# Kernel optimization log

Measured on AMD Instinct MI355X. Metric: run time of the kernel, lower is better.

The kernel has to match this reference:

```python
import jax, jax.numpy as jnp
import numpy as np

B, Nq, Nk, R = 4, 1024, 1024, 256
NH, DK, DV = 8, 64, 64


def setup_inputs() -> dict:
    key = jax.random.key(0)
    ks = jax.random.split(key, 16)
    mk = lambda k, shape, s=1.0: jax.random.normal(k, shape, dtype=jnp.float32) * s
    inp = {
        'Q_real': mk(ks[0], (B, Nq, R)), 'Q_imag': mk(ks[1], (B, Nq, R)),
        'K_real': mk(ks[2], (B, Nk, R)), 'K_imag': mk(ks[3], (B, Nk, R)),
        'V_real': mk(ks[4], (B, Nk, R)), 'V_imag': mk(ks[5], (B, Nk, R)),
        'WQ_r': mk(ks[6], (NH * DK, R), 0.02), 'WQ_i': mk(ks[7], (NH * DK, R), 0.02),
        'WK_r': mk(ks[8], (NH * DK, R), 0.02), 'WK_i': mk(ks[9], (NH * DK, R), 0.02),
        'WV_r': mk(ks[10], (NH * DV, R), 0.02), 'WV_i': mk(ks[11], (NH * DV, R), 0.02),
        'WO_r': mk(ks[12], (R, NH * DV), 0.02), 'WO_i': mk(ks[13], (R, NH * DV), 0.02),
        'mask': jax.random.randint(ks[14], (B, Nk), 0, 2).astype(bool),
    }
    return inp


def _complex_linear(x, w_r, w_i):
    # x: complex [..., in]; weights real [out, in]. Same math as 4 real matmuls.
    w = (w_r + 1j * w_i).astype(jnp.complex64)
    return x @ w.T


def reference(Q_real, Q_imag, K_real, K_imag, V_real, V_imag,
              WQ_r, WQ_i, WK_r, WK_i, WV_r, WV_i, WO_r, WO_i, mask):
    Q = (Q_real + 1j * Q_imag).astype(jnp.complex64)
    K = (K_real + 1j * K_imag).astype(jnp.complex64)
    V = (V_real + 1j * V_imag).astype(jnp.complex64)

    Qp = _complex_linear(Q, WQ_r, WQ_i).reshape(B, Nq, NH, DK).transpose(0, 2, 1, 3)
    Kp = _complex_linear(K, WK_r, WK_i).reshape(B, Nk, NH, DK).transpose(0, 2, 1, 3)
    Vp = _complex_linear(V, WV_r, WV_i).reshape(B, Nk, NH, DV).transpose(0, 2, 1, 3)

    # complex scores [B, NH, Nq, Nk]; conj on K matches torch .conj().transpose
    scores = jnp.einsum('bhqd,bhkd->bhqk', Qp, jnp.conj(Kp)) / jnp.sqrt(jnp.float32(DK))
    scores_abs = jnp.abs(scores)

    m = mask[:, None, None, :]                    # [B,1,1,Nk]
    valid = jnp.any(mask, axis=-1)[:, None, None, None]  # [B,1,1,1] valid query rows
    masked = jnp.where(m, scores_abs, -jnp.inf)
    # avoid all -inf rows feeding softmax (those rows are zeroed afterwards)
    safe = jnp.where(valid, masked, 0.0)
    w = jax.nn.softmax(safe, axis=-1)
    w = jnp.where(valid, w, 0.0)

    attn = jnp.einsum('bhqk,bhkd->bhqd', w.astype(Vp.dtype), Vp)
    attn = attn.transpose(0, 2, 1, 3).reshape(B, Nq, NH * DV)
    return _complex_linear(attn, WO_r, WO_i)
```

## Files before the change

kernel.cpp:

```cpp
#include <hip/hip_runtime.h>
#include <math.h>

#define NBATCH 4
#define NSEQ   1024
#define RD     256
#define NHEAD  8
#define HD     64
#define NHD    512

typedef __attribute__((ext_vector_type(8))) short  short8;
typedef __attribute__((ext_vector_type(4))) short  short4v;
typedef __attribute__((ext_vector_type(4))) float  float4v;

#define MFMA16(a,b,c) __builtin_amdgcn_mfma_f32_16x16x32_bf16(a,b,c,0,0,0)

typedef const void __attribute__((address_space(1)))* gas_t;
typedef void __attribute__((address_space(3)))* las_t;
#define GLOAD16(g, l) __builtin_amdgcn_global_load_lds((gas_t)(g), (las_t)(l), 16, 0, 0)

static __device__ __forceinline__ unsigned short f2b(float f) {
    union { float f; unsigned u; } x; x.f = f;
    unsigned r = x.u + 0x7fffu + ((x.u >> 16) & 1u);
    return (unsigned short)(r >> 16);
}
static __device__ __forceinline__ void st4(short* dst, float4v v) {
    short4v p;
    p[0] = (short)f2b(v[0]); p[1] = (short)f2b(v[1]);
    p[2] = (short)f2b(v[2]); p[3] = (short)f2b(v[3]);
    *(short4v*)dst = p;
}

__global__ __launch_bounds__(1024) void mask_norm(
    const void* __restrict__ mraw, unsigned char* __restrict__ nm)
{
    __shared__ int isByteLayout;
    const int t = threadIdx.x;
    if (t == 0) isByteLayout = 0;
    __syncthreads();
    const int* mi = (const int*)mraw;
    int v = mi[t];
    if (v & ~1) isByteLayout = 1;
    __syncthreads();
    const unsigned char* mb = (const unsigned char*)mraw;
    if (isByteLayout) {
        #pragma unroll
        for (int j = 0; j < 4; j++) { int k = t*4 + j; nm[k] = mb[k] ? 1 : 0; }
    } else {
        #pragma unroll
        for (int j = 0; j < 4; j++) { int k = t*4 + j; nm[k] = mi[k] ? 1 : 0; }
    }
}

struct ConvArgs { const float* src[14]; short* dst[14]; int n4[14]; };

__global__ __launch_bounds__(256) void convert_bf16(ConvArgs ca)
{
    const int a = blockIdx.y;
    const float* __restrict__ s = ca.src[a];
    short* __restrict__ d = ca.dst[a];
    const int n4 = ca.n4[a];
    for (int i = blockIdx.x*256 + threadIdx.x; i < n4; i += gridDim.x*256) {
        float4v v = *(const float4v*)(s + (size_t)i*4);
        st4(d + (size_t)i*4, v);
    }
}

struct ProjArgs {
    const short* Xr[3]; const short* Xi[3];
    const short* Wr[3]; const short* Wi[3];
    short* Yr[3]; short* Yi[3];
};

__global__ __launch_bounds__(256) void cgemm_proj(ProjArgs pa)
{
    __shared__ short sX[2][64][64];
    __shared__ short sW[2][64][64];
    const int z = blockIdx.z;
    const short* __restrict__ X_r = pa.Xr[z];
    const short* __restrict__ X_i = pa.Xi[z];
    const short* __restrict__ W_r = pa.Wr[z];
    const short* __restrict__ W_i = pa.Wi[z];
    short* __restrict__ Y_r = pa.Yr[z];
    short* __restrict__ Y_i = pa.Yi[z];
    const int transposeOut = (z == 2);

    const int tid  = threadIdx.x;
    const int lane = tid & 63, wave = tid >> 6;
    const int quad = lane >> 4, l16 = lane & 15;
    const int sw8  = l16 & 7;
    const int rsub = lane >> 3;
    const int colg = (lane & 7) ^ rsub;
    const int n0 = blockIdx.x * 64, m0 = blockIdx.y * 64;

    const short nk = (short)0x8000;
    const short8 neg = {nk,nk,nk,nk,nk,nk,nk,nk};

    float4v zf = {0.f,0.f,0.f,0.f};
    float4v Yr[4], Yi[4];
    #pragma unroll
    for (int t = 0; t < 4; t++) { Yr[t] = zf; Yi[t] = zf; }

    for (int kc = 0; kc < RD; kc += 64) {
        __syncthreads();
        {
            const short* gp; short* lp; int rbase;
            if      (wave == 0) { gp = X_r; lp = &sX[0][0][0]; rbase = m0; }
            else if (wave == 1) { gp = X_i; lp = &sX[1][0][0]; rbase = m0; }
            else if (wave == 2) { gp = W_r; lp = &sW[0][0][0]; rbase = n0; }
            else                { gp = W_i; lp = &sW[1][0][0]; rbase = n0; }
            #pragma unroll
            for (int j = 0; j < 8; j++) {
                int row = j*8 + rsub;
                GLOAD16(gp + (size_t)(rbase + row)*RD + kc + colg*8, lp + j*512);
            }
        }
        __syncthreads();
        short8 fxr[2], fxi[2], fxin[2];
        #pragma unroll
        for (int ds = 0; ds < 2; ds++) {
            int u = ((ds*4 + quad) ^ sw8) * 8;
            fxr[ds]  = *(short8*)&sX[0][wave*16 + l16][u];
            fxi[ds]  = *(short8*)&sX[1][wave*16 + l16][u];
            fxin[ds] = fxi[ds] ^ neg;
        }
        #pragma unroll
        for (int t = 0; t < 4; t++)
            #pragma unroll
            for (int ds = 0; ds < 2; ds++) {
                int u = ((ds*4 + quad) ^ sw8) * 8;
                short8 wr = *(short8*)&sW[0][t*16 + l16][u];
                short8 wi = *(short8*)&sW[1][t*16 + l16][u];
                Yr[t] = MFMA16(fxr[ds],  wr, Yr[t]);
                Yr[t] = MFMA16(fxin[ds], wi, Yr[t]);
                Yi[t] = MFMA16(fxr[ds],  wi, Yi[t]);
                Yi[t] = MFMA16(fxi[ds],  wr, Yi[t]);
            }
    }

    const int b = m0 >> 10, h = n0 >> 6, nb = m0 & 1023;
    short* sT = &sX[0][0][0];
    short* Yp[2] = { Y_r, Y_i };
    #pragma unroll
    for (int p = 0; p < 2; p++) {
        __syncthreads();
        #pragma unroll
        for (int t = 0; t < 4; t++)
            #pragma unroll
            for (int r = 0; r < 4; r++) {
                float v = p ? Yi[t][r] : Yr[t][r];
                int rr = wave*16 + quad*4 + r;
                int cc = t*16 + l16;
                if (!transposeOut) sT[rr*68 + cc] = (short)f2b(v);
                else               sT[cc*68 + rr] = (short)f2b(v);
            }
        __syncthreads();
        #pragma unroll
        for (int it = 0; it < 2; it++) {
            int idx = it*256 + tid;
            int rr = idx >> 3, c8 = (idx & 7)*8;
            short4v a = *(short4v*)&sT[rr*68 + c8];
            short4v bq = *(short4v*)&sT[rr*68 + c8 + 4];
            short8 v8 = { a[0],a[1],a[2],a[3], bq[0],bq[1],bq[2],bq[3] };
            size_t o = transposeOut
                ? (((size_t)(b*NHEAD + h))*HD + rr)*NSEQ + nb + c8
                : (((size_t)(b*NHEAD + h))*NSEQ + nb + rr)*HD + c8;
            *(short8*)&Yp[p][o] = v8;
        }
    }
}

__global__ __launch_bounds__(256) void attn_mfma(
    const short* __restrict__ Qp_r, const short* __restrict__ Qp_i,
    const short* __restrict__ Kp_r, const short* __restrict__ Kp_i,
    const short* __restrict__ Vp_r, const short* __restrict__ Vp_i,
    const unsigned char* __restrict__ mask,
    short* __restrict__ Ar, short* __restrict__ Ai)
{
    __shared__ short sK[2][64][64];
    __shared__ short sV[2][64][64];
    __shared__ short sP[4][16][72];
    __shared__ unsigned char smask[1024];

    const int tid  = threadIdx.x;
    const int lane = tid & 63, wave = tid >> 6;
    const int quad = lane >> 4, l16 = lane & 15;
    const int sw8  = l16 & 7;
    const int qt = blockIdx.x & 15;
    const int bh = blockIdx.x >> 4;
    const int b  = bh >> 3, h = bh & 7;
    const size_t base = (size_t)bh * (NSEQ*HD);

    const int rsub = lane >> 3;
    const int colg = (lane & 7) ^ rsub;

    ((int*)smask)[tid] = ((const int*)(mask + b*NSEQ))[tid];

    {
        const int q0 = qt*64;
        #pragma unroll
        for (int j = 0; j < 4; j++) {
            int c = wave*4 + j;
            const short* gp = (c >> 3) ? Qp_i : Qp_r;
            short* lp = (c >> 3) ? &sK[1][0][0] : &sK[0][0][0];
            int jj = c & 7;
            int row = jj*8 + rsub;
            GLOAD16(gp + base + (size_t)(q0 + row)*HD + colg*8, lp + jj*512);
        }
    }
    __syncthreads();

    short8 fqr[2], fqi[2], fqrn[2];
    {
        const short nk = (short)0x8000;
        short8 neg = {nk,nk,nk,nk,nk,nk,nk,nk};
        const int qrow = wave*16 + l16;
        #pragma unroll
        for (int ds = 0; ds < 2; ds++) {
            int u = ((ds*4 + quad) ^ sw8) * 8;
            fqr[ds]  = *(short8*)&sK[0][qrow][u];
            fqi[ds]  = *(short8*)&sK[1][qrow][u];
            fqrn[ds] = fqr[ds] ^ neg;
        }
    }

    float4v zf = {0.f,0.f,0.f,0.f};
    float4v Or[4], Oi[4];
    float lrow[4];
    #pragma unroll
    for (int t = 0; t < 4; t++) { Or[t] = zf; Oi[t] = zf; }
    #pragma unroll
    for (int r = 0; r < 4; r++) lrow[r] = 0.f;

    const float C2 = 0.18033688f;

    for (int kt = 0; kt < 16; kt++) {
        const int k0 = kt*64;
        __syncthreads();
        {
            const short* gp; short* lp; int isV;
            if      (wave == 0) { gp = Kp_r; lp = &sK[0][0][0]; isV = 0; }
            else if (wave == 1) { gp = Kp_i; lp = &sK[1][0][0]; isV = 0; }
            else if (wave == 2) { gp = Vp_r; lp = &sV[0][0][0]; isV = 1; }
            else                { gp = Vp_i; lp = &sV[1][0][0]; isV = 1; }
            #pragma unroll
            for (int j = 0; j < 8; j++) {
                int row = j*8 + rsub;
                const short* g = isV
                    ? gp + base + (size_t)row*NSEQ + k0 + colg*8
                    : gp + base + (size_t)(k0 + row)*HD + colg*8;
                GLOAD16(g, lp + j*512);
            }
        }
        __syncthreads();

        float4v Sr[4], Si[4];
        #pragma unroll
        for (int t = 0; t < 4; t++) { Sr[t] = zf; Si[t] = zf; }
        #pragma unroll
        for (int t = 0; t < 4; t++)
            #pragma unroll
            for (int ds = 0; ds < 2; ds++) {
                int u = ((ds*4 + quad) ^ sw8) * 8;
                short8 kr = *(short8*)&sK[0][t*16 + l16][u];
                short8 ki = *(short8*)&sK[1][t*16 + l16][u];
                Sr[t] = MFMA16(fqr[ds],  kr, Sr[t]);
                Sr[t] = MFMA16(fqi[ds],  ki, Sr[t]);
                Si[t] = MFMA16(fqi[ds],  kr, Si[t]);
                Si[t] = MFMA16(fqrn[ds], ki, Si[t]);
            }

        #pragma unroll
        for (int t = 0; t < 4; t++) {
            bool mv = smask[k0 + t*16 + l16] != 0;
            #pragma unroll
            for (int r = 0; r < 4; r++) {
                float a = Sr[t][r], c = Si[t][r];
                float x = fmaf(a, a, c*c);
                float s = __builtin_amdgcn_sqrtf(x);
                float e = mv ? __builtin_amdgcn_exp2f(C2 * s) : 0.f;
                lrow[r] += e;
                sP[wave][quad*4 + r][t*16 + l16] = (short)f2b(e);
            }
        }

        #pragma unroll
        for (int ks = 0; ks < 2; ks++) {
            short8 fp = *(short8*)&sP[wave][l16][ks*32 + quad*8];
            #pragma unroll
            for (int t = 0; t < 4; t++) {
                int u = ((ks*4 + quad) ^ sw8) * 8;
                short8 vr = *(short8*)&sV[0][t*16 + l16][u];
                short8 vi = *(short8*)&sV[1][t*16 + l16][u];
                Or[t] = MFMA16(fp, vr, Or[t]);
                Oi[t] = MFMA16(fp, vi, Oi[t]);
            }
        }
    }

    float inv[4];
    #pragma unroll
    for (int r = 0; r < 4; r++) {
        float ls = lrow[r];
        ls += __shfl_xor(ls, 1, 64);
        ls += __shfl_xor(ls, 2, 64);
        ls += __shfl_xor(ls, 4, 64);
        ls += __shfl_xor(ls, 8, 64);
        inv[r] = (ls > 0.f) ? 1.f/ls : 0.f;
    }
    #pragma unroll
    for (int t = 0; t < 4; t++)
        #pragma unroll
        for (int r = 0; r < 4; r++) {
            int q = qt*64 + wave*16 + quad*4 + r;
            int d = t*16 + l16;
            size_t o = ((size_t)(b*NSEQ + q))*NHD + h*HD + d;
            Ar[o] = (short)f2b(Or[t][r] * inv[r]);
            Ai[o] = (short)f2b(Oi[t][r] * inv[r]);
        }
}

__global__ __launch_bounds__(256) void cgemm_out(
    const short* __restrict__ A_r, const short* __restrict__ A_i,
    const short* __restrict__ W_r, const short* __restrict__ W_i,
    float* __restrict__ Out, int writeImagPlane)
{
    __shared__ short sA[2][64][64];
    __shared__ short sW[2][32][64];
    const int tid  = threadIdx.x;
    const int lane = tid & 63, wave = tid >> 6;
    const int quad = lane >> 4, l16 = lane & 15;
    const int sw8  = l16 & 7;
    const int rsub = lane >> 3;
    const int colg = (lane & 7) ^ rsub;
    const int n0 = blockIdx.x * 32, m0 = blockIdx.y * 64;

    const short nk = (short)0x8000;
    const short8 neg = {nk,nk,nk,nk,nk,nk,nk,nk};

    float4v zf = {0.f,0.f,0.f,0.f};
    float4v Yr[2], Yi[2];
    #pragma unroll
    for (int t = 0; t < 2; t++) { Yr[t] = zf; Yi[t] = zf; }

    for (int kc = 0; kc < NHD; kc += 64) {
        __syncthreads();
        {
            if (wave < 2) {
                const short* gp = wave ? A_i : A_r;
                short* lp = wave ? &sA[1][0][0] : &sA[0][0][0];
                #pragma unroll
                for (int j = 0; j < 8; j++) {
                    int row = j*8 + rsub;
                    GLOAD16(gp + (size_t)(m0 + row)*NHD + kc + colg*8, lp + j*512);
                }
            } else {
                const short* gp = (wave == 3) ? W_i : W_r;
                short* lp = (wave == 3) ? &sW[1][0][0] : &sW[0][0][0];
                #pragma unroll
                for (int j = 0; j < 4; j++) {
                    int row = j*8 + rsub;
                    GLOAD16(gp + (size_t)(n0 + row)*NHD + kc + colg*8, lp + j*512);
                }
            }
        }
        __syncthreads();
        short8 far[2], fai[2], fain[2];
        #pragma unroll
        for (int ds = 0; ds < 2; ds++) {
            int u = ((ds*4 + quad) ^ sw8) * 8;
            far[ds]  = *(short8*)&sA[0][wave*16 + l16][u];
            fai[ds]  = *(short8*)&sA[1][wave*16 + l16][u];
            fain[ds] = fai[ds] ^ neg;
        }
        #pragma unroll
        for (int t = 0; t < 2; t++)
            #pragma unroll
            for (int ds = 0; ds < 2; ds++) {
                int u = ((ds*4 + quad) ^ sw8) * 8;
                short8 wr = *(short8*)&sW[0][t*16 + l16][u];
                short8 wi = *(short8*)&sW[1][t*16 + l16][u];
                Yr[t] = MFMA16(far[ds],  wr, Yr[t]);
                Yr[t] = MFMA16(fain[ds], wi, Yr[t]);
                Yi[t] = MFMA16(far[ds],  wi, Yi[t]);
                Yi[t] = MFMA16(fai[ds],  wr, Yi[t]);
            }
    }
    const size_t TOT = (size_t)NBATCH * NSEQ * RD;
    #pragma unroll
    for (int t = 0; t < 2; t++)
        #pragma unroll
        for (int r = 0; r < 4; r++) {
            int row = m0 + wave*16 + quad*4 + r;
            int col = n0 + t*16 + l16;
            size_t o = (size_t)row*RD + col;
            Out[o] = Yr[t][r];
            if (writeImagPlane) Out[o + TOT] = Yi[t][r];
        }
}

extern "C" void kernel_launch(void* const* d_in, const int* in_sizes, int n_in,
                              void* d_out, int out_size, void* d_ws, size_t ws_size,
                              hipStream_t stream)
{
    float* out = (float*)d_out;

    const size_t P = (size_t)NBATCH * NHEAD * NSEQ * HD;
    const size_t H = (size_t)NBATCH * NSEQ * RD;
    const size_t WSZ = (size_t)NHD * RD;

    short* bws = (short*)d_ws;
    short* Qpr = bws + 0*P;  short* Qpi = bws + 1*P;
    short* Kpr = bws + 2*P;  short* Kpi = bws + 3*P;
    short* Vpr = bws + 4*P;  short* Vpi = bws + 5*P;
    short* conv = bws + 6*P;
    short* cX[6]; for (int i = 0; i < 6; i++) cX[i] = conv + i*H;
    short* cW[6]; for (int i = 0; i < 6; i++) cW[i] = conv + 6*H + i*WSZ;
    short* cWOr = conv + 6*H + 6*WSZ;
    short* cWOi = conv + 6*H + 7*WSZ;
    short* Apr = conv;
    short* Api = conv + P;
    unsigned char* nmask = (unsigned char*)(conv + 6*H + 8*WSZ);

    const size_t TOT = (size_t)NBATCH * NSEQ * RD;
    const int writeImagPlane = ((size_t)out_size >= 2*TOT) ? 1 : 0;

    ConvArgs ca;
    for (int i = 0; i < 6; i++) {
        ca.src[i] = (const float*)d_in[i];  ca.dst[i] = cX[i];  ca.n4[i] = (int)(H/4);
    }
    for (int i = 0; i < 6; i++) {
        ca.src[6+i] = (const float*)d_in[6+i]; ca.dst[6+i] = cW[i]; ca.n4[6+i] = (int)(WSZ/4);
    }
    ca.src[12] = (const float*)d_in[12]; ca.dst[12] = cWOr; ca.n4[12] = (int)(WSZ/4);
    ca.src[13] = (const float*)d_in[13]; ca.dst[13] = cWOi; ca.n4[13] = (int)(WSZ/4);

    ProjArgs pa;
    pa.Xr[0] = cX[0]; pa.Xi[0] = cX[1];
    pa.Xr[1] = cX[2]; pa.Xi[1] = cX[3];
    pa.Xr[2] = cX[4]; pa.Xi[2] = cX[5];
    pa.Wr[0] = cW[0]; pa.Wi[0] = cW[1];
    pa.Wr[1] = cW[2]; pa.Wi[1] = cW[3];
    pa.Wr[2] = cW[4]; pa.Wi[2] = cW[5];
    pa.Yr[0] = Qpr; pa.Yi[0] = Qpi;
    pa.Yr[1] = Kpr; pa.Yi[1] = Kpi;
    pa.Yr[2] = Vpr; pa.Yi[2] = Vpi;

    mask_norm<<<1, 1024, 0, stream>>>(d_in[14], nmask);
    convert_bf16<<<dim3(256, 14), 256, 0, stream>>>(ca);
    cgemm_proj<<<dim3(8, 64, 3), 256, 0, stream>>>(pa);
    attn_mfma<<<dim3(512), 256, 0, stream>>>(Qpr, Qpi, Kpr, Kpi, Vpr, Vpi,
                                             nmask, Apr, Api);
    cgemm_out<<<dim3(8, 64), 256, 0, stream>>>(Apr, Api, cWOr, cWOi, out,
                                               writeImagPlane);
}
```

Before: 176.3 us.

## Fold mask normalization into convert kernel, enlarge projection M-tile, reorder attention blocks

Removes the separate mask_norm launch by handling the mask as an extra y-slice of convert_bf16, saving one kernel launch. The projection GEMM now uses 128-row M tiles, with each wave computing two 16-row sub-tiles, so every loaded W tile is reused twice and the grid is halved. The attention grid mapping is reordered so consecutive blocks cover different batch-heads rather than query tiles of the same head. The larger GEMM tile raises register and LDS use and lowers block count, which may reduce occupancy.

New measurement: 175.4 us. No clear change (-0.5%).

```diff
diff --git a/kernel.cpp b/kernel.cpp
--- a/kernel.cpp
+++ b/kernel.cpp
@@ -30,32 +30,35 @@
     *(short4v*)dst = p;
 }
 
-__global__ __launch_bounds__(1024) void mask_norm(
-    const void* __restrict__ mraw, unsigned char* __restrict__ nm)
-{
-    __shared__ int isByteLayout;
-    const int t = threadIdx.x;
-    if (t == 0) isByteLayout = 0;
-    __syncthreads();
-    const int* mi = (const int*)mraw;
-    int v = mi[t];
-    if (v & ~1) isByteLayout = 1;
-    __syncthreads();
-    const unsigned char* mb = (const unsigned char*)mraw;
-    if (isByteLayout) {
-        #pragma unroll
-        for (int j = 0; j < 4; j++) { int k = t*4 + j; nm[k] = mb[k] ? 1 : 0; }
-    } else {
-        #pragma unroll
-        for (int j = 0; j < 4; j++) { int k = t*4 + j; nm[k] = mi[k] ? 1 : 0; }
-    }
-}
-
-struct ConvArgs { const float* src[14]; short* dst[14]; int n4[14]; };
+struct ConvArgs { const float* src[15]; short* dst[15]; int n4[15]; };
 
 __global__ __launch_bounds__(256) void convert_bf16(ConvArgs ca)
 {
     const int a = blockIdx.y;
+    if (a == 14) {
+        if (blockIdx.x != 0) return;
+        __shared__ int isByteLayout;
+        const int t = threadIdx.x;
+        if (t == 0) isByteLayout = 0;
+        __syncthreads();
+        const int* mi = (const int*)ca.src[14];
+        #pragma unroll
+        for (int j = 0; j < 4; j++) {
+            int v = mi[t*4 + j];
+            if (v & ~1) isByteLayout = 1;
+        }
+        __syncthreads();
+        unsigned char* nm = (unsigned char*)ca.dst[14];
+        const unsigned char* mb = (const unsigned char*)ca.src[14];
+        if (isByteLayout) {
+            #pragma unroll
+            for (int j = 0; j < 16; j++) { int k = t*16 + j; nm[k] = mb[k] ? 1 : 0; }
+        } else {
+            #pragma unroll
+            for (int j = 0; j < 16; j++) { int k = t*16 + j; nm[k] = mi[k] ? 1 : 0; }
+        }
+        return;
+    }
     const float* __restrict__ s = ca.src[a];
     short* __restrict__ d = ca.dst[a];
     const int n4 = ca.n4[a];
@@ -73,7 +76,7 @@
 
 __global__ __launch_bounds__(256) void cgemm_proj(ProjArgs pa)
 {
-    __shared__ short sX[2][64][64];
+    __shared__ short sX[2][128][64];
     __shared__ short sW[2][64][64];
     const int z = blockIdx.z;
     const short* __restrict__ X_r = pa.Xr[z];
@@ -90,39 +93,49 @@
     const int sw8  = l16 & 7;
     const int rsub = lane >> 3;
     const int colg = (lane & 7) ^ rsub;
-    const int n0 = blockIdx.x * 64, m0 = blockIdx.y * 64;
+    const int n0 = blockIdx.x * 64, m0 = blockIdx.y * 128;
 
     const short nk = (short)0x8000;
     const short8 neg = {nk,nk,nk,nk,nk,nk,nk,nk};
 
     float4v zf = {0.f,0.f,0.f,0.f};
-    float4v Yr[4], Yi[4];
-    #pragma unroll
-    for (int t = 0; t < 4; t++) { Yr[t] = zf; Yi[t] = zf; }
+    float4v Yr[2][4], Yi[2][4];
+    #pragma unroll
+    for (int ms = 0; ms < 2; ms++)
+        #pragma unroll
+        for (int t = 0; t < 4; t++) { Yr[ms][t] = zf; Yi[ms][t] = zf; }
 
     for (int kc = 0; kc < RD; kc += 64) {
         __syncthreads();
-        {
-            const short* gp; short* lp; int rbase;
-            if      (wave == 0) { gp = X_r; lp = &sX[0][0][0]; rbase = m0; }
-            else if (wave == 1) { gp = X_i; lp = &sX[1][0][0]; rbase = m0; }
-            else if (wave == 2) { gp = W_r; lp = &sW[0][0][0]; rbase = n0; }
-            else                { gp = W_i; lp = &sW[1][0][0]; rbase = n0; }
+        if (wave < 2) {
+            const short* gp = wave ? X_i : X_r;
+            short* lp = wave ? &sX[1][0][0] : &sX[0][0][0];
+            #pragma unroll
+            for (int j = 0; j < 16; j++) {
+                int row = j*8 + rsub;
+                GLOAD16(gp + (size_t)(m0 + row)*RD + kc + colg*8, lp + j*512);
+            }
+        } else {
+            const short* gp = (wave == 3) ? W_i : W_r;
+            short* lp = (wave == 3) ? &sW[1][0][0] : &sW[0][0][0];
             #pragma unroll
             for (int j = 0; j < 8; j++) {
                 int row = j*8 + rsub;
-                GLOAD16(gp + (size_t)(rbase + row)*RD + kc + colg*8, lp + j*512);
-            }
-        }
-        __syncthreads();
-        short8 fxr[2], fxi[2], fxin[2];
-        #pragma unroll
-        for (int ds = 0; ds < 2; ds++) {
-            int u = ((ds*4 + quad) ^ sw8) * 8;
-            fxr[ds]  = *(short8*)&sX[0][wave*16 + l16][u];
-            fxi[ds]  = *(short8*)&sX[1][wave*16 + l16][u];
-            fxin[ds] = fxi[ds] ^ neg;
-        }
+                GLOAD16(gp + (size_t)(n0 + row)*RD + kc + colg*8, lp + j*512);
+            }
+        }
+        __syncthreads();
+        short8 fxr[2][2], fxi[2][2], fxin[2][2];
+        #pragma unroll
+        for (int ms = 0; ms < 2; ms++)
+            #pragma unroll
+            for (int ds = 0; ds < 2; ds++) {
+                int row = wave*32 + ms*16 + l16;
+                int u = ((ds*4 + quad) ^ sw8) * 8;
+                fxr[ms][ds]  = *(short8*)&sX[0][row][u];
+                fxi[ms][ds]  = *(short8*)&sX[1][row][u];
+                fxin[ms][ds] = fxi[ms][ds] ^ neg;
+            }
         #pragma unroll
         for (int t = 0; t < 4; t++)
             #pragma unroll
@@ -130,10 +143,13 @@
                 int u = ((ds*4 + quad) ^ sw8) * 8;
                 short8 wr = *(short8*)&sW[0][t*16 + l16][u];
                 short8 wi = *(short8*)&sW[1][t*16 + l16][u];
-                Yr[t] = MFMA16(fxr[ds],  wr, Yr[t]);
-                Yr[t] = MFMA16(fxin[ds], wi, Yr[t]);
-                Yi[t] = MFMA16(fxr[ds],  wi, Yi[t]);
-                Yi[t] = MFMA16(fxi[ds],  wr, Yi[t]);
+                #pragma unroll
+                for (int ms = 0; ms < 2; ms++) {
+                    Yr[ms][t] = MFMA16(fxr[ms][ds],  wr, Yr[ms][t]);
+                    Yr[ms][t] = MFMA16(fxin[ms][ds], wi, Yr[ms][t]);
+                    Yi[ms][t] = MFMA16(fxr[ms][ds],  wi, Yi[ms][t]);
+                    Yi[ms][t] = MFMA16(fxi[ms][ds],  wr, Yi[ms][t]);
+                }
             }
     }
 
@@ -144,26 +160,36 @@
     for (int p = 0; p < 2; p++) {
         __syncthreads();
         #pragma unroll
-        for (int t = 0; t < 4; t++)
-            #pragma unroll
-            for (int r = 0; r < 4; r++) {
-                float v = p ? Yi[t][r] : Yr[t][r];
-                int rr = wave*16 + quad*4 + r;
-                int cc = t*16 + l16;
-                if (!transposeOut) sT[rr*68 + cc] = (short)f2b(v);
-                else               sT[cc*68 + rr] = (short)f2b(v);
-            }
-        __syncthreads();
-        #pragma unroll
-        for (int it = 0; it < 2; it++) {
+        for (int ms = 0; ms < 2; ms++)
+            #pragma unroll
+            for (int t = 0; t < 4; t++)
+                #pragma unroll
+                for (int r = 0; r < 4; r++) {
+                    float v = p ? Yi[ms][t][r] : Yr[ms][t][r];
+                    int rr = wave*32 + ms*16 + quad*4 + r;
+                    int cc = t*16 + l16;
+                    if (!transposeOut) sT[rr*68 + cc]  = (short)f2b(v);
+                    else               sT[cc*132 + rr] = (short)f2b(v);
+                }
+        __syncthreads();
+        #pragma unroll
+        for (int it = 0; it < 4; it++) {
             int idx = it*256 + tid;
-            int rr = idx >> 3, c8 = (idx & 7)*8;
-            short4v a = *(short4v*)&sT[rr*68 + c8];
-            short4v bq = *(short4v*)&sT[rr*68 + c8 + 4];
+            int rr, c8;
+            size_t o;
+            const short* sp;
+            if (!transposeOut) {
+                rr = idx >> 3; c8 = (idx & 7)*8;
+                sp = &sT[rr*68 + c8];
+                o = (((size_t)(b*NHEAD + h))*NSEQ + nb + rr)*HD + c8;
+            } else {
+                rr = idx >> 4; c8 = (idx & 15)*8;
+                sp = &sT[rr*132 + c8];
+                o = (((size_t)(b*NHEAD + h))*HD + rr)*NSEQ + nb + c8;
+            }
+            short4v a = *(short4v*)sp;
+            short4v bq = *(short4v*)(sp + 4);
             short8 v8 = { a[0],a[1],a[2],a[3], bq[0],bq[1],bq[2],bq[3] };
-            size_t o = transposeOut
-                ? (((size_t)(b*NHEAD + h))*HD + rr)*NSEQ + nb + c8
-                : (((size_t)(b*NHEAD + h))*NSEQ + nb + rr)*HD + c8;
             *(short8*)&Yp[p][o] = v8;
         }
     }
@@ -185,8 +211,8 @@
     const int lane = tid & 63, wave = tid >> 6;
     const int quad = lane >> 4, l16 = lane & 15;
     const int sw8  = l16 & 7;
-    const int qt = blockIdx.x & 15;
-    const int bh = blockIdx.x >> 4;
+    const int qt = blockIdx.x >> 5;
+    const int bh = blockIdx.x & 31;
     const int b  = bh >> 3, h = bh & 7;
     const size_t base = (size_t)bh * (NSEQ*HD);
 
@@ -433,6 +459,7 @@
     }
     ca.src[12] = (const float*)d_in[12]; ca.dst[12] = cWOr; ca.n4[12] = (int)(WSZ/4);
     ca.src[13] = (const float*)d_in[13]; ca.dst[13] = cWOi; ca.n4[13] = (int)(WSZ/4);
+    ca.src[14] = (const float*)d_in[14]; ca.dst[14] = (short*)nmask; ca.n4[14] = 0;
 
     ProjArgs pa;
     pa.Xr[0] = cX[0]; pa.Xi[0] = cX[1];
@@ -445,9 +472,8 @@
     pa.Yr[1] = Kpr; pa.Yi[1] = Kpi;
     pa.Yr[2] = Vpr; pa.Yi[2] = Vpi;
 
-    mask_norm<<<1, 1024, 0, stream>>>(d_in[14], nmask);
-    convert_bf16<<<dim3(256, 14), 256, 0, stream>>>(ca);
-    cgemm_proj<<<dim3(8, 64, 3), 256, 0, stream>>>(pa);
+    convert_bf16<<<dim3(256, 15), 256, 0, stream>>>(ca);
+    cgemm_proj<<<dim3(8, 32, 3), 256, 0, stream>>>(pa);
     attn_mfma<<<dim3(512), 256, 0, stream>>>(Qpr, Qpi, Kpr, Kpi, Vpr, Vpi,
                                              nmask, Apr, Api);
     cgemm_out<<<dim3(8, 64), 256, 0, stream>>>(Apr, Api, cWOr, cWOi, out,
```
